# Kernel tuning notes

Hardware: AMD Instinct MI355X
Metric: run time of the kernel (lower is better)

Reference implementation:

```python
import jax, jax.numpy as jnp
import numpy as np

T, B, D, H, L, O = 800, 32, 440, 1024, 4, 2000
EPS = 1e-5

def _bn(x, g, b, m, v):
    return (x - m) * jax.lax.rsqrt(v + EPS) * g + b

def setup_inputs() -> dict:
    key = jax.random.key(0)
    ks = jax.random.split(key, 12)
    s = 0.02
    return {
        "xs": jax.random.normal(ks[0], (T, B, D), dtype=jnp.float32),
        "w0": jax.random.normal(ks[1], (2 * H, D), dtype=jnp.float32) * s,
        "wr": jax.random.normal(ks[2], (L - 1, 2 * H, H), dtype=jnp.float32) * s,
        "bnz_g": jnp.ones((L, H), jnp.float32),
        "bnz_b": jnp.zeros((L, H), jnp.float32),
        "bnz_m": jax.random.normal(ks[3], (L, H), dtype=jnp.float32) * 0.1,
        "bnz_v": jax.random.uniform(ks[4], (L, H), dtype=jnp.float32) + 0.5,
        "bnc_g": jnp.ones((L, H), jnp.float32),
        "bnc_b": jnp.zeros((L, H), jnp.float32),
        "bnc_m": jax.random.normal(ks[5], (L, H), dtype=jnp.float32) * 0.1,
        "bnc_v": jax.random.uniform(ks[6], (L, H), dtype=jnp.float32) + 0.5,
        "wf": jax.random.normal(ks[7], (O, H), dtype=jnp.float32) * 0.003,
        "bnf_g": jnp.ones((O,), jnp.float32),
        "bnf_b": jnp.zeros((O,), jnp.float32),
        "bnf_m": jax.random.normal(ks[8], (O,), dtype=jnp.float32) * 0.1,
        "bnf_v": jax.random.uniform(ks[9], (O,), dtype=jnp.float32) + 0.5,
    }

def reference(xs, w0, wr, bnz_g, bnz_b, bnz_m, bnz_v, bnc_g, bnc_b, bnc_m, bnc_v, wf, bnf_g, bnf_b, bnf_m, bnf_v):
    x = xs  # [T,B,feat]
    for i in range(L):
        W = w0 if i == 0 else wr[i - 1]
        ws = jnp.einsum('tbd,hd->tbh', x, W)          # [T,B,2H]
        wz, wc = jnp.split(ws, 2, axis=-1)
        z = jax.nn.sigmoid(_bn(wz, bnz_g[i], bnz_b[i], bnz_m[i], bnz_v[i]))
        c = jax.nn.relu(_bn(wc, bnc_g[i], bnc_b[i], bnc_m[i], bnc_v[i]))
        def step(h, zc):
            z_t, c_t = zc
            h = (1.0 - z_t) * c_t + z_t * h
            return h, h
        _, hs = jax.lax.scan(step, jnp.zeros((B, H), x.dtype), (z, c))
        x = hs  # [T,B,H]
    out = jnp.einsum('tbh,oh->tbo', x, wf).reshape(T * B, O)
    out = _bn(out, bnf_g, bnf_b, bnf_m, bnf_v)
    return jax.nn.log_softmax(out, axis=1)
```

## Files before the change

kernel.cpp:

```cpp
#include <hip/hip_runtime.h>
#include <math.h>
#include <stdint.h>

#define T_ 800
#define B_ 32
#define D_ 440
#define DP_ 448
#define H_ 1024
#define L_ 4
#define O_ 2000
#define OP_ 2048
#define EPS_ 1e-5f
#define M_ (T_ * B_)
#define BH_ (B_ * H_)
#define NC_ 16
#define TC_ (T_ / NC_)

#define BM2 256
#define BN2 256
#define BK2 64

typedef __attribute__((ext_vector_type(8))) short bf16x8;
typedef __attribute__((ext_vector_type(4))) float f32x4;

__device__ inline float b2f(unsigned short u) {
    union { unsigned int i; float f; } v; v.i = ((unsigned int)u) << 16; return v.f;
}
__device__ inline unsigned short f2b(float f) {
    unsigned int x = __float_as_uint(f);
    return (unsigned short)((x + 0x7FFFu + ((x >> 16) & 1u)) >> 16);
}

__global__ void bn_prep(const float* __restrict__ g, const float* __restrict__ b,
                        const float* __restrict__ m, const float* __restrict__ v,
                        float* __restrict__ scale, float* __restrict__ bias,
                        int nsrc, int ndst)
{
    int i = blockIdx.x * 256 + threadIdx.x;
    if (i >= ndst) return;
    if (i < nsrc) {
        float s = g[i] * rsqrtf(v[i] + EPS_);
        scale[i] = s;
        bias[i] = fmaf(-m[i], s, b[i]);
    } else {
        scale[i] = 0.f;
        bias[i] = 0.f;
    }
}

__global__ void cvt_pad8(const float* __restrict__ src, unsigned short* __restrict__ dst,
                         int Rs, int Cs, int Cd, int total8)
{
    int i = blockIdx.x * 256 + threadIdx.x;
    if (i >= total8) return;
    const int c8 = Cd >> 3;
    int r = i / c8, c = (i - r * c8) << 3;
    ushort4 lo, hi;
    if (r < Rs && c < Cs) {
        const float4 a = *(const float4*)(src + (size_t)r * Cs + c);
        const float4 b = *(const float4*)(src + (size_t)r * Cs + c + 4);
        lo = make_ushort4(f2b(a.x), f2b(a.y), f2b(a.z), f2b(a.w));
        hi = make_ushort4(f2b(b.x), f2b(b.y), f2b(b.z), f2b(b.w));
    } else {
        lo = make_ushort4(0, 0, 0, 0);
        hi = make_ushort4(0, 0, 0, 0);
    }
    unsigned short* d = dst + (size_t)r * Cd + c;
    *(ushort4*)d = lo;
    *(ushort4*)(d + 4) = hi;
}


#define GLDS16(src, dst) __builtin_amdgcn_global_load_lds( \
    (const __attribute__((address_space(1))) unsigned int*)(src), \
    (__attribute__((address_space(3))) unsigned int*)(dst), 16, 0, 0)

#define SBAR() __builtin_amdgcn_s_barrier()
#define LGKM0() do { asm volatile("s_waitcnt lgkmcnt(0)" ::: "memory"); \
                     __builtin_amdgcn_sched_barrier(0); } while (0)

__global__ __launch_bounds__(512, 2) void gemm_bf16(
    const unsigned short* __restrict__ A, const unsigned short* __restrict__ Wt,
    int K, int mode,
    unsigned short* __restrict__ zout, unsigned short* __restrict__ cout,
    const float* __restrict__ zscale, const float* __restrict__ zbias,
    const float* __restrict__ cscale, const float* __restrict__ cbias,
    unsigned short* __restrict__ fout,
    const float* __restrict__ fscale, const float* __restrict__ fbias)
{
    __shared__ unsigned short As[2][2][128 * 64];
    __shared__ unsigned short Bs[2][2][128 * 64];

    const int tid = threadIdx.x;
    const int lane = tid & 63;
    const int wid = tid >> 6;
    const int wm = wid >> 2;
    const int wn = wid & 3;
    const int wn1 = wn & 1;

    const int bx = blockIdx.x & 7;
    const int by = blockIdx.x >> 3;
    const int m0 = by * BM2;
    const int n0 = bx * BN2;

    const int rl0 = (wid * 2 + 0) * 8 + (lane >> 3);
    const int rl1 = (wid * 2 + 1) * 8 + (lane >> 3);
    const int cswz = ((lane & 7) * 8) ^ ((lane >> 3) << 3);

    const unsigned short* aS00 = A + (size_t)(m0 + rl0) * K + cswz;
    const unsigned short* aS01 = A + (size_t)(m0 + rl1) * K + cswz;
    const unsigned short* aS10 = A + (size_t)(m0 + 128 + rl0) * K + cswz;
    const unsigned short* aS11 = A + (size_t)(m0 + 128 + rl1) * K + cswz;

    const int gc00 = n0 + ((rl0 >> 6) << 6) + (rl0 & 15) * 4 + ((rl0 >> 4) & 3);
    const int gc01 = n0 + ((rl1 >> 6) << 6) + (rl1 & 15) * 4 + ((rl1 >> 4) & 3);
    const int s10 = 128 + rl0, s11 = 128 + rl1;
    const int gc10 = n0 + ((s10 >> 6) << 6) + (s10 & 15) * 4 + ((s10 >> 4) & 3);
    const int gc11 = n0 + ((s11 >> 6) << 6) + (s11 & 15) * 4 + ((s11 >> 4) & 3);
    const unsigned short* bS00 = Wt + (size_t)gc00 * K + cswz;
    const unsigned short* bS01 = Wt + (size_t)gc01 * K + cswz;
    const unsigned short* bS10 = Wt + (size_t)gc10 * K + cswz;
    const unsigned short* bS11 = Wt + (size_t)gc11 * K + cswz;

    const int ls0 = (wid * 2 + 0) * 512;
    const int ls1 = (wid * 2 + 1) * 512;

    const int fr = lane & 15;
    const int q = lane >> 4;
    const int rxor = (fr & 7) << 3;
    const int c0 = (q * 8) ^ rxor;
    const int c1 = (32 + q * 8) ^ rxor;

    f32x4 acc[8][4];
    #pragma unroll
    for (int i = 0; i < 8; i++)
        #pragma unroll
        for (int j = 0; j < 4; j++)
            acc[i][j] = (f32x4){0.f, 0.f, 0.f, 0.f};

    bf16x8 af[4][2];
    bf16x8 bfv[4][2];

    const int nT = K / BK2;

    GLDS16(aS00, &As[0][0][ls0]); GLDS16(aS01, &As[0][0][ls1]);
    GLDS16(aS10, &As[0][1][ls0]); GLDS16(aS11, &As[0][1][ls1]);
    GLDS16(bS00, &Bs[0][0][ls0]); GLDS16(bS01, &Bs[0][0][ls1]);
    GLDS16(bS10, &Bs[0][1][ls0]); GLDS16(bS11, &Bs[0][1][ls1]);
    if (nT > 1) {
        GLDS16(bS00 + BK2, &Bs[1][0][ls0]); GLDS16(bS01 + BK2, &Bs[1][0][ls1]);
        GLDS16(aS00 + BK2, &As[1][0][ls0]); GLDS16(aS01 + BK2, &As[1][0][ls1]);
    }
    asm volatile("s_waitcnt vmcnt(4)" ::: "memory");
    SBAR();

#define READ_A(MOFF) do { _Pragma("unroll") \
    for (int m_ = 0; m_ < 4; ++m_) { \
        af[m_][0] = *(const bf16x8*)(Ac + ((MOFF + m_) * 16 + fr) * 64 + c0); \
        af[m_][1] = *(const bf16x8*)(Ac + ((MOFF + m_) * 16 + fr) * 64 + c1); \
    } } while (0)

#define READ_B(NOFF) do { _Pragma("unroll") \
    for (int n_ = 0; n_ < 2; ++n_) { \
        bfv[NOFF + n_][0] = *(const bf16x8*)(Bc + (wn1 * 64 + (NOFF + n_) * 16 + fr) * 64 + c0); \
        bfv[NOFF + n_][1] = *(const bf16x8*)(Bc + (wn1 * 64 + (NOFF + n_) * 16 + fr) * 64 + c1); \
    } } while (0)

#define MFMA16(MBASE, NBASE) do { \
    __builtin_amdgcn_s_setprio(1); \
    _Pragma("unroll") \
    for (int m_ = 0; m_ < 4; ++m_) \
        _Pragma("unroll") \
        for (int n_ = 0; n_ < 2; ++n_) \
            _Pragma("unroll") \
            for (int ks_ = 0; ks_ < 2; ++ks_) \
                acc[MBASE + m_][NBASE + n_] = __builtin_amdgcn_mfma_f32_16x16x32_bf16( \
                    af[m_][ks_], bfv[NBASE + n_][ks_], acc[MBASE + m_][NBASE + n_], 0, 0, 0); \
    __builtin_amdgcn_s_setprio(0); \
} while (0)

    for (int t = 0; t < nT; ++t) {
        const int cur = t & 1, nxt = cur ^ 1;
        const unsigned short* Ac = &As[cur][wm][0];
        const unsigned short* Bc = &Bs[cur][wn >> 1][0];
        const int k1 = (t + 1) * BK2;
        const int k2 = (t + 2) * BK2;

        READ_A(0);
        READ_B(0);
        if (t + 1 < nT) {
            GLDS16(aS10 + k1, &As[nxt][1][ls0]);
            GLDS16(aS11 + k1, &As[nxt][1][ls1]);
        }
        SBAR();
        LGKM0();
        MFMA16(0, 0);
        SBAR();

        READ_B(2);
        if (t + 1 < nT) {
            GLDS16(bS10 + k1, &Bs[nxt][1][ls0]);
            GLDS16(bS11 + k1, &Bs[nxt][1][ls1]);
        }
        SBAR();
        LGKM0();
        MFMA16(0, 2);
        SBAR();

        READ_A(4);
        if (t + 2 < nT) {
            GLDS16(bS00 + k2, &Bs[cur][0][ls0]);
            GLDS16(bS01 + k2, &Bs[cur][0][ls1]);
        }
        SBAR();
        LGKM0();
        MFMA16(4, 2);
        SBAR();

        if (t + 2 < nT) {
            GLDS16(aS00 + k2, &As[cur][0][ls0]);
            GLDS16(aS01 + k2, &As[cur][0][ls1]);
        }
        SBAR();
        MFMA16(4, 0);
        if (t + 2 < nT) {
            asm volatile("s_waitcnt vmcnt(4)" ::: "memory");
        } else {
            asm volatile("s_waitcnt vmcnt(0)" ::: "memory");
        }
        SBAR();
    }

#undef READ_A
#undef READ_B
#undef MFMA16

    const int colb = n0 + wn * 64 + fr * 4;
    const int rbase = m0 + wm * 128 + q * 4;

    if (mode == 0) {
        const bool isz = (n0 < H_);
        const float* sc = isz ? zscale : cscale;
        const float* bi = isz ? zbias : cbias;
        unsigned short* dst = isz ? zout : cout;
        const int npb = isz ? colb : colb - H_;
        const float4 s4 = *(const float4*)(sc + npb);
        const float4 b4 = *(const float4*)(bi + npb);
        #pragma unroll
        for (int m = 0; m < 8; ++m)
            #pragma unroll
            for (int r = 0; r < 4; ++r) {
                const int mm = rbase + m * 16 + r;
                float v0 = fmaf(acc[m][0][r], s4.x, b4.x);
                float v1 = fmaf(acc[m][1][r], s4.y, b4.y);
                float v2 = fmaf(acc[m][2][r], s4.z, b4.z);
                float v3 = fmaf(acc[m][3][r], s4.w, b4.w);
                if (isz) {
                    v0 = __builtin_amdgcn_rcpf(1.f + __expf(-v0));
                    v1 = __builtin_amdgcn_rcpf(1.f + __expf(-v1));
                    v2 = __builtin_amdgcn_rcpf(1.f + __expf(-v2));
                    v3 = __builtin_amdgcn_rcpf(1.f + __expf(-v3));
                } else {
                    v0 = fmaxf(v0, 0.f); v1 = fmaxf(v1, 0.f);
                    v2 = fmaxf(v2, 0.f); v3 = fmaxf(v3, 0.f);
                }
                ushort4 pk = make_ushort4(f2b(v0), f2b(v1), f2b(v2), f2b(v3));
                *(ushort4*)(dst + (size_t)mm * H_ + npb) = pk;
            }
    } else {
        const float4 s4 = *(const float4*)(fscale + colb);
        const float4 b4 = *(const float4*)(fbias + colb);
        #pragma unroll
        for (int m = 0; m < 8; ++m)
            #pragma unroll
            for (int r = 0; r < 4; ++r) {
                const int mm = rbase + m * 16 + r;
                ushort4 pk = make_ushort4(
                    f2b(fmaf(acc[m][0][r], s4.x, b4.x)),
                    f2b(fmaf(acc[m][1][r], s4.y, b4.y)),
                    f2b(fmaf(acc[m][2][r], s4.z, b4.z)),
                    f2b(fmaf(acc[m][3][r], s4.w, b4.w)));
                *(ushort4*)(fout + (size_t)mm * OP_ + colb) = pk;
            }
    }
}

__global__ __launch_bounds__(256) void scan_pass1(
    const unsigned short* __restrict__ z, const unsigned short* __restrict__ c,
    float* __restrict__ H0, float* __restrict__ P)
{
    const int k = blockIdx.y;
    const int e2 = blockIdx.x * 256 + threadIdx.x;
    float h0 = 0.f, h1 = 0.f, p0 = 1.f, p1 = 1.f;
    size_t off = ((size_t)k * TC_ * BH_ + 2 * e2) >> 1;
    const unsigned int* z32 = (const unsigned int*)z;
    const unsigned int* c32 = (const unsigned int*)c;
    #pragma unroll 5
    for (int t = 0; t < TC_; ++t) {
        unsigned int zz = z32[off], cc = c32[off];
        float z0 = b2f((unsigned short)zz), z1 = b2f((unsigned short)(zz >> 16));
        float c0 = b2f((unsigned short)cc), c1 = b2f((unsigned short)(cc >> 16));
        h0 = fmaf(z0, h0 - c0, c0);  p0 *= z0;
        h1 = fmaf(z1, h1 - c1, c1);  p1 *= z1;
        off += BH_ / 2;
    }
    *(float2*)(H0 + (size_t)k * BH_ + 2 * e2) = make_float2(h0, h1);
    *(float2*)(P  + (size_t)k * BH_ + 2 * e2) = make_float2(p0, p1);
}

__global__ __launch_bounds__(256) void scan_pass2(
    const unsigned short* __restrict__ z, const unsigned short* __restrict__ c,
    const float* __restrict__ H0, const float* __restrict__ P,
    unsigned short* __restrict__ x)
{
    const int k = blockIdx.y;
    const int e2 = blockIdx.x * 256 + threadIdx.x;
    float h0 = 0.f, h1 = 0.f;
    for (int j = 0; j < k; ++j) {
        float2 pj = *(const float2*)(P  + (size_t)j * BH_ + 2 * e2);
        float2 hj = *(const float2*)(H0 + (size_t)j * BH_ + 2 * e2);
        h0 = fmaf(pj.x, h0, hj.x);
        h1 = fmaf(pj.y, h1, hj.y);
    }
    size_t off = ((size_t)k * TC_ * BH_ + 2 * e2) >> 1;
    const unsigned int* z32 = (const unsigned int*)z;
    const unsigned int* c32 = (const unsigned int*)c;
    unsigned int* x32 = (unsigned int*)x;
    #pragma unroll 5
    for (int t = 0; t < TC_; ++t) {
        unsigned int zz = z32[off], cc = c32[off];
        float z0 = b2f((unsigned short)zz), z1 = b2f((unsigned short)(zz >> 16));
        float c0 = b2f((unsigned short)cc), c1 = b2f((unsigned short)(cc >> 16));
        h0 = fmaf(z0, h0 - c0, c0);
        h1 = fmaf(z1, h1 - c1, c1);
        x32[off] = (unsigned int)f2b(h0) | ((unsigned int)f2b(h1) << 16);
        off += BH_ / 2;
    }
}

__global__ __launch_bounds__(256) void logsoftmax_kernel(
    const unsigned short* __restrict__ lg, float* __restrict__ out)
{
    const int row = blockIdx.x;
    const unsigned short* p = lg + (size_t)row * OP_;
    float* po = out + (size_t)row * O_;
    const int tid = threadIdx.x;

    float v[8];
    float mx = -1e30f;
    #pragma unroll
    for (int j = 0; j < 8; j++) {
        int col = tid + j * 256;
        v[j] = (col < O_) ? b2f(p[col]) : -1e30f;
        mx = fmaxf(mx, v[j]);
    }
    #pragma unroll
    for (int o = 32; o > 0; o >>= 1) mx = fmaxf(mx, __shfl_down(mx, o));
    __shared__ float smax[4];
    __shared__ float ssum[4];
    const int lane = tid & 63, wid = tid >> 6;
    if (lane == 0) smax[wid] = mx;
    __syncthreads();
    mx = fmaxf(fmaxf(smax[0], smax[1]), fmaxf(smax[2], smax[3]));

    float s = 0.f;
    #pragma unroll
    for (int j = 0; j < 8; j++) {
        int col = tid + j * 256;
        if (col < O_) s += expf(v[j] - mx);
    }
    #pragma unroll
    for (int o = 32; o > 0; o >>= 1) s += __shfl_down(s, o);
    if (lane == 0) ssum[wid] = s;
    __syncthreads();
    s = ssum[0] + ssum[1] + ssum[2] + ssum[3];
    const float lse = mx + logf(s);

    #pragma unroll
    for (int j = 0; j < 8; j++) {
        int col = tid + j * 256;
        if (col < O_) po[col] = v[j] - lse;
    }
}

extern "C" void kernel_launch(void* const* d_in, const int* in_sizes, int n_in,
                              void* d_out, int out_size, void* d_ws, size_t ws_size,
                              hipStream_t stream)
{
    (void)in_sizes; (void)n_in; (void)out_size; (void)ws_size;

    const float* xs    = (const float*)d_in[0];
    const float* w0    = (const float*)d_in[1];
    const float* wr    = (const float*)d_in[2];
    const float* bnz_g = (const float*)d_in[3];
    const float* bnz_b = (const float*)d_in[4];
    const float* bnz_m = (const float*)d_in[5];
    const float* bnz_v = (const float*)d_in[6];
    const float* bnc_g = (const float*)d_in[7];
    const float* bnc_b = (const float*)d_in[8];
    const float* bnc_m = (const float*)d_in[9];
    const float* bnc_v = (const float*)d_in[10];
    const float* wf    = (const float*)d_in[11];
    const float* bnf_g = (const float*)d_in[12];
    const float* bnf_b = (const float*)d_in[13];
    const float* bnf_m = (const float*)d_in[14];
    const float* bnf_v = (const float*)d_in[15];
    float* out = (float*)d_out;

    unsigned short* p = (unsigned short*)d_ws;
    unsigned short* xbuf  = p;  p += (size_t)M_ * H_;
    unsigned short* x0buf = p;  p += (size_t)M_ * DP_;
    unsigned short* zbuf  = p;  p += (size_t)M_ * H_;
    unsigned short* cbuf  = p;  p += (size_t)M_ * H_;
    unsigned short* w0p   = p;  p += (size_t)(2 * H_) * DP_;
    unsigned short* wrp   = p;  p += (size_t)(L_ - 1) * (2 * H_) * H_;
    unsigned short* wfp   = p;  p += (size_t)OP_ * H_;
    unsigned short* lbuf  = p;  p += (size_t)M_ * OP_;
    float* fp = (float*)p;
    float* zs = fp;  fp += L_ * H_;
    float* zb = fp;  fp += L_ * H_;
    float* cs = fp;  fp += L_ * H_;
    float* cb = fp;  fp += L_ * H_;
    float* fs = fp;  fp += OP_;
    float* fb = fp;  fp += OP_;
    float* sH0 = fp; fp += NC_ * BH_;
    float* sP  = fp;

    dim3 blk(256);
    bn_prep<<<(L_ * H_ + 255) / 256, blk, 0, stream>>>(bnz_g, bnz_b, bnz_m, bnz_v, zs, zb, L_ * H_, L_ * H_);
    bn_prep<<<(L_ * H_ + 255) / 256, blk, 0, stream>>>(bnc_g, bnc_b, bnc_m, bnc_v, cs, cb, L_ * H_, L_ * H_);
    bn_prep<<<(OP_ + 255) / 256, blk, 0, stream>>>(bnf_g, bnf_b, bnf_m, bnf_v, fs, fb, O_, OP_);

    {
        int t0 = M_ * DP_ / 8;
        cvt_pad8<<<(t0 + 255) / 256, blk, 0, stream>>>(xs, x0buf, M_, D_, DP_, t0);
        int t1 = 2 * H_ * DP_ / 8;
        cvt_pad8<<<(t1 + 255) / 256, blk, 0, stream>>>(w0, w0p, 2 * H_, D_, DP_, t1);
        int t2 = (L_ - 1) * 2 * H_ * H_ / 8;
        cvt_pad8<<<(t2 + 255) / 256, blk, 0, stream>>>(wr, wrp, (L_ - 1) * 2 * H_, H_, H_, t2);
        int t3 = OP_ * H_ / 8;
        cvt_pad8<<<(t3 + 255) / 256, blk, 0, stream>>>(wf, wfp, O_, H_, H_, t3);
    }

    dim3 blk2(512);
    dim3 grid2((M_ / BM2) * ((2 * H_) / BN2));
    dim3 sgrid1(BH_ / 512, NC_ - 1);
    dim3 sgrid2(BH_ / 512, NC_);
    for (int layer = 0; layer < L_; ++layer) {
        const unsigned short* Ain = (layer == 0) ? x0buf : xbuf;
        const unsigned short* W   = (layer == 0) ? w0p : (wrp + (size_t)(layer - 1) * (2 * H_) * H_);
        const int K               = (layer == 0) ? DP_ : H_;
        gemm_bf16<<<grid2, blk2, 0, stream>>>(Ain, W, K, 0,
            zbuf, cbuf,
            zs + layer * H_, zb + layer * H_, cs + layer * H_, cb + layer * H_,
            nullptr, nullptr, nullptr);
        scan_pass1<<<sgrid1, blk, 0, stream>>>(zbuf, cbuf, sH0, sP);
        scan_pass2<<<sgrid2, blk, 0, stream>>>(zbuf, cbuf, sH0, sP, xbuf);
    }

    dim3 gridf((M_ / BM2) * (OP_ / BN2));
    gemm_bf16<<<gridf, blk2, 0, stream>>>(xbuf, wfp, H_, 1,
        nullptr, nullptr, nullptr, nullptr, nullptr, nullptr,
        lbuf, fs, fb);

    logsoftmax_kernel<<<M_, blk, 0, stream>>>(lbuf, out);
}
```

Measured before the change: 1.140 ms.

## Restructure bf16 GEMM to 128x256 tiles with 4 waves and BK=32

Shrinks the GEMM block tile from 256x256x64 with 8 waves to 128x256x32 with 4 waves. Each wave now owns a 128x64 output slice and the LDS layout is rewritten to drop the XOR swizzle, with a simplified two-phase pipeline that uses fewer barriers per k-step. The aim is more blocks for better CU occupancy and load balance, plus less LDS use and fewer synchronisations. In exchange, each loaded byte is reused less, and removing the swizzle may introduce LDS bank conflicts.

```diff
diff --git a/kernel.cpp b/kernel.cpp
--- a/kernel.cpp
+++ b/kernel.cpp
@@ -16,9 +16,9 @@
 #define NC_ 16
 #define TC_ (T_ / NC_)
 
-#define BM2 256
+#define BM2 128
 #define BN2 256
-#define BK2 64
+#define BK2 32
 
 typedef __attribute__((ext_vector_type(8))) short bf16x8;
 typedef __attribute__((ext_vector_type(4))) float f32x4;
@@ -79,7 +79,7 @@
 #define LGKM0() do { asm volatile("s_waitcnt lgkmcnt(0)" ::: "memory"); \
                      __builtin_amdgcn_sched_barrier(0); } while (0)
 
-__global__ __launch_bounds__(512, 2) void gemm_bf16(
+__global__ __launch_bounds__(256, 2) void gemm_bf16(
     const unsigned short* __restrict__ A, const unsigned short* __restrict__ Wt,
     int K, int mode,
     unsigned short* __restrict__ zout, unsigned short* __restrict__ cout,
@@ -88,48 +88,38 @@
     unsigned short* __restrict__ fout,
     const float* __restrict__ fscale, const float* __restrict__ fbias)
 {
-    __shared__ unsigned short As[2][2][128 * 64];
-    __shared__ unsigned short Bs[2][2][128 * 64];
+    __shared__ unsigned short As[2][128 * 32];
+    __shared__ unsigned short Bs[2][256 * 32];
 
     const int tid = threadIdx.x;
     const int lane = tid & 63;
     const int wid = tid >> 6;
-    const int wm = wid >> 2;
-    const int wn = wid & 3;
-    const int wn1 = wn & 1;
 
     const int bx = blockIdx.x & 7;
     const int by = blockIdx.x >> 3;
     const int m0 = by * BM2;
     const int n0 = bx * BN2;
 
-    const int rl0 = (wid * 2 + 0) * 8 + (lane >> 3);
-    const int rl1 = (wid * 2 + 1) * 8 + (lane >> 3);
-    const int cswz = ((lane & 7) * 8) ^ ((lane >> 3) << 3);
-
-    const unsigned short* aS00 = A + (size_t)(m0 + rl0) * K + cswz;
-    const unsigned short* aS01 = A + (size_t)(m0 + rl1) * K + cswz;
-    const unsigned short* aS10 = A + (size_t)(m0 + 128 + rl0) * K + cswz;
-    const unsigned short* aS11 = A + (size_t)(m0 + 128 + rl1) * K + cswz;
-
-    const int gc00 = n0 + ((rl0 >> 6) << 6) + (rl0 & 15) * 4 + ((rl0 >> 4) & 3);
-    const int gc01 = n0 + ((rl1 >> 6) << 6) + (rl1 & 15) * 4 + ((rl1 >> 4) & 3);
-    const int s10 = 128 + rl0, s11 = 128 + rl1;
-    const int gc10 = n0 + ((s10 >> 6) << 6) + (s10 & 15) * 4 + ((s10 >> 4) & 3);
-    const int gc11 = n0 + ((s11 >> 6) << 6) + (s11 & 15) * 4 + ((s11 >> 4) & 3);
-    const unsigned short* bS00 = Wt + (size_t)gc00 * K + cswz;
-    const unsigned short* bS01 = Wt + (size_t)gc01 * K + cswz;
-    const unsigned short* bS10 = Wt + (size_t)gc10 * K + cswz;
-    const unsigned short* bS11 = Wt + (size_t)gc11 * K + cswz;
-
-    const int ls0 = (wid * 2 + 0) * 512;
-    const int ls1 = (wid * 2 + 1) * 512;
+    const int srow = lane >> 2;
+    const int scol = (lane & 3) * 8;
+
+    const unsigned short* aE = A + (size_t)(m0 + wid * 16 + srow) * K + scol;
+    const unsigned short* aL = A + (size_t)(m0 + 64 + wid * 16 + srow) * K + scol;
+    const unsigned short* bS0 = Wt + (size_t)(n0 + wid * 64 + srow * 4 + 0) * K + scol;
+    const unsigned short* bS1 = Wt + (size_t)(n0 + wid * 64 + srow * 4 + 1) * K + scol;
+    const unsigned short* bS2 = Wt + (size_t)(n0 + wid * 64 + srow * 4 + 2) * K + scol;
+    const unsigned short* bS3 = Wt + (size_t)(n0 + wid * 64 + srow * 4 + 3) * K + scol;
+
+    const int lsAE = wid * 512;
+    const int lsAL = (4 + wid) * 512;
+    const int lsB0 = (wid * 4 + 0) * 512;
+    const int lsB1 = (wid * 4 + 1) * 512;
+    const int lsB2 = (wid * 4 + 2) * 512;
+    const int lsB3 = (wid * 4 + 3) * 512;
 
     const int fr = lane & 15;
     const int q = lane >> 4;
-    const int rxor = (fr & 7) << 3;
-    const int c0 = (q * 8) ^ rxor;
-    const int c1 = (32 + q * 8) ^ rxor;
+    const int rdc = q * 8;
 
     f32x4 acc[8][4];
     #pragma unroll
@@ -138,105 +128,86 @@
         for (int j = 0; j < 4; j++)
             acc[i][j] = (f32x4){0.f, 0.f, 0.f, 0.f};
 
-    bf16x8 af[4][2];
-    bf16x8 bfv[4][2];
+    bf16x8 af[4], bfv[4];
 
     const int nT = K / BK2;
 
-    GLDS16(aS00, &As[0][0][ls0]); GLDS16(aS01, &As[0][0][ls1]);
-    GLDS16(aS10, &As[0][1][ls0]); GLDS16(aS11, &As[0][1][ls1]);
-    GLDS16(bS00, &Bs[0][0][ls0]); GLDS16(bS01, &Bs[0][0][ls1]);
-    GLDS16(bS10, &Bs[0][1][ls0]); GLDS16(bS11, &Bs[0][1][ls1]);
+    GLDS16(aE,  &As[0][lsAE]);
+    GLDS16(bS0, &Bs[0][lsB0]); GLDS16(bS1, &Bs[0][lsB1]);
+    GLDS16(bS2, &Bs[0][lsB2]); GLDS16(bS3, &Bs[0][lsB3]);
+    GLDS16(aL,  &As[0][lsAL]);
     if (nT > 1) {
-        GLDS16(bS00 + BK2, &Bs[1][0][ls0]); GLDS16(bS01 + BK2, &Bs[1][0][ls1]);
-        GLDS16(aS00 + BK2, &As[1][0][ls0]); GLDS16(aS01 + BK2, &As[1][0][ls1]);
-    }
-    asm volatile("s_waitcnt vmcnt(4)" ::: "memory");
+        GLDS16(aE + BK2,  &As[1][lsAE]);
+        GLDS16(bS0 + BK2, &Bs[1][lsB0]); GLDS16(bS1 + BK2, &Bs[1][lsB1]);
+        GLDS16(bS2 + BK2, &Bs[1][lsB2]); GLDS16(bS3 + BK2, &Bs[1][lsB3]);
+        asm volatile("s_waitcnt vmcnt(6)" ::: "memory");
+    } else {
+        asm volatile("s_waitcnt vmcnt(1)" ::: "memory");
+    }
     SBAR();
 
-#define READ_A(MOFF) do { _Pragma("unroll") \
-    for (int m_ = 0; m_ < 4; ++m_) { \
-        af[m_][0] = *(const bf16x8*)(Ac + ((MOFF + m_) * 16 + fr) * 64 + c0); \
-        af[m_][1] = *(const bf16x8*)(Ac + ((MOFF + m_) * 16 + fr) * 64 + c1); \
-    } } while (0)
-
-#define READ_B(NOFF) do { _Pragma("unroll") \
-    for (int n_ = 0; n_ < 2; ++n_) { \
-        bfv[NOFF + n_][0] = *(const bf16x8*)(Bc + (wn1 * 64 + (NOFF + n_) * 16 + fr) * 64 + c0); \
-        bfv[NOFF + n_][1] = *(const bf16x8*)(Bc + (wn1 * 64 + (NOFF + n_) * 16 + fr) * 64 + c1); \
-    } } while (0)
-
-#define MFMA16(MBASE, NBASE) do { \
+#define MFMA16(MBASE) do { \
     __builtin_amdgcn_s_setprio(1); \
     _Pragma("unroll") \
     for (int m_ = 0; m_ < 4; ++m_) \
         _Pragma("unroll") \
-        for (int n_ = 0; n_ < 2; ++n_) \
-            _Pragma("unroll") \
-            for (int ks_ = 0; ks_ < 2; ++ks_) \
-                acc[MBASE + m_][NBASE + n_] = __builtin_amdgcn_mfma_f32_16x16x32_bf16( \
-                    af[m_][ks_], bfv[NBASE + n_][ks_], acc[MBASE + m_][NBASE + n_], 0, 0, 0); \
+        for (int n_ = 0; n_ < 4; ++n_) \
+            acc[MBASE + m_][n_] = __builtin_amdgcn_mfma_f32_16x16x32_bf16( \
+                af[m_], bfv[n_], acc[MBASE + m_][n_], 0, 0, 0); \
     __builtin_amdgcn_s_setprio(0); \
 } while (0)
 
     for (int t = 0; t < nT; ++t) {
         const int cur = t & 1, nxt = cur ^ 1;
-        const unsigned short* Ac = &As[cur][wm][0];
-        const unsigned short* Bc = &Bs[cur][wn >> 1][0];
-        const int k1 = (t + 1) * BK2;
-        const int k2 = (t + 2) * BK2;
-
-        READ_A(0);
-        READ_B(0);
+        const unsigned short* Ac = As[cur];
+        const unsigned short* Bc = Bs[cur] + wid * (64 * 32);
+        const int kL = (t + 1) * BK2;
+        const int kE = (t + 2) * BK2;
+
+        #pragma unroll
+        for (int m_ = 0; m_ < 4; ++m_)
+            af[m_] = *(const bf16x8*)(Ac + (m_ * 16 + fr) * 32 + rdc);
+        #pragma unroll
+        for (int n_ = 0; n_ < 4; ++n_)
+            bfv[n_] = *(const bf16x8*)(Bc + (n_ * 16 + fr) * 32 + rdc);
         if (t + 1 < nT) {
-            GLDS16(aS10 + k1, &As[nxt][1][ls0]);
-            GLDS16(aS11 + k1, &As[nxt][1][ls1]);
+            GLDS16(aL + kL, &As[nxt][lsAL]);
         }
         SBAR();
         LGKM0();
-        MFMA16(0, 0);
-        SBAR();
-
-        READ_B(2);
+        MFMA16(0);
         if (t + 1 < nT) {
-            GLDS16(bS10 + k1, &Bs[nxt][1][ls0]);
-            GLDS16(bS11 + k1, &Bs[nxt][1][ls1]);
-        }
-        SBAR();
-        LGKM0();
-        MFMA16(0, 2);
-        SBAR();
-
-        READ_A(4);
-        if (t + 2 < nT) {
-            GLDS16(bS00 + k2, &Bs[cur][0][ls0]);
-            GLDS16(bS01 + k2, &Bs[cur][0][ls1]);
-        }
-        SBAR();
-        LGKM0();
-        MFMA16(4, 2);
-        SBAR();
-
-        if (t + 2 < nT) {
-            GLDS16(aS00 + k2, &As[cur][0][ls0]);
-            GLDS16(aS01 + k2, &As[cur][0][ls1]);
-        }
-        SBAR();
-        MFMA16(4, 0);
-        if (t + 2 < nT) {
-            asm volatile("s_waitcnt vmcnt(4)" ::: "memory");
+            asm volatile("s_waitcnt vmcnt(6)" ::: "memory");
         } else {
             asm volatile("s_waitcnt vmcnt(0)" ::: "memory");
         }
         SBAR();
-    }
-
-#undef READ_A
-#undef READ_B
+
+        #pragma unroll
+        for (int m_ = 0; m_ < 4; ++m_)
+            af[m_] = *(const bf16x8*)(Ac + ((4 + m_) * 16 + fr) * 32 + rdc);
+        if (t + 2 < nT) {
+            GLDS16(aE + kE,  &As[cur][lsAE]);
+            GLDS16(bS0 + kE, &Bs[cur][lsB0]); GLDS16(bS1 + kE, &Bs[cur][lsB1]);
+            GLDS16(bS2 + kE, &Bs[cur][lsB2]); GLDS16(bS3 + kE, &Bs[cur][lsB3]);
+        }
+        SBAR();
+        LGKM0();
+        MFMA16(4);
+        if (t + 2 < nT) {
+            asm volatile("s_waitcnt vmcnt(6)" ::: "memory");
+        } else if (t + 1 < nT) {
+            asm volatile("s_waitcnt vmcnt(1)" ::: "memory");
+        } else {
+            asm volatile("s_waitcnt vmcnt(0)" ::: "memory");
+        }
+        SBAR();
+    }
+
 #undef MFMA16
 
-    const int colb = n0 + wn * 64 + fr * 4;
-    const int rbase = m0 + wm * 128 + q * 4;
+    const int colb = n0 + wid * 64 + fr * 4;
+    const int rbase = m0 + q * 4;
 
     if (mode == 0) {
         const bool isz = (n0 < H_);
@@ -442,7 +413,7 @@
         cvt_pad8<<<(t3 + 255) / 256, blk, 0, stream>>>(wf, wfp, O_, H_, H_, t3);
     }
 
-    dim3 blk2(512);
+    dim3 blk2(256);
     dim3 grid2((M_ / BM2) * ((2 * H_) / BN2));
     dim3 sgrid1(BH_ / 512, NC_ - 1);
     dim3 sgrid2(BH_ / 512, NC_);
```

After: 1.121 ms. Within noise of the previous version (-1.6%).
